# Kernel tuning notes

Hardware: AMD Instinct MI355X
Metric: run time of the kernel (lower is better)

## Reference

```python
import jax, jax.numpy as jnp
import numpy as np
import math

N_CELLS = 2048; HC_DIM = 11; HC_NODES = 2048
D = 1024; IN_DIM = 512; L = 2; H = 8; B = 2; HD = D // H
# XOR neighbor table: hypercube scatter-to-neighbor == gather-from-neighbor (involution)
NBR_WALK = jnp.asarray(np.arange(HC_NODES)[:, None] ^ (1 << np.arange(HC_DIM)))  # [Nn, hc_dim]
NB_INJ = min(HC_DIM, 6)
NB_FRUST = min(int(math.log2(N_CELLS)), 10)
FRUST_BITS = jnp.asarray(1 << np.arange(NB_FRUST))
N_MORPH = 48; N_FRUST_SAMPLES = min(N_CELLS, 128)


def _walk_step(amps, coin, x_mean):
    coined = jnp.einsum('ij,njd->nid', coin, amps)              # [Nn,2,D] complex
    new1 = coined[:, 1, :][NBR_WALK].sum(1) / HC_DIM            # XOR neighbor mix
    new = jnp.stack([coined[:, 0, :], new1], axis=1)
    new = new * jnp.exp(1j * (x_mean * 0.1))
    return new / (jnp.sqrt((jnp.abs(new) ** 2).sum()) + 1e-8)


def _inject(cells, amps):
    probs = (jnp.abs(amps) ** 2).sum((1, 2))
    probs = probs / (probs.sum() + 1e-8)
    ph = jnp.angle(amps.sum(1)).mean(-1)                        # [Nn]
    idx = jnp.arange(N_CELLS) % HC_NODES
    p = probs[idx]
    phc = ph[idx] * 0.3
    cells = cells * (0.8 + 0.4 * p)[:, None]
    c, s = jnp.cos(phc)[:, None], jnp.sin(phc)[:, None]
    h1, h2 = cells[:, :D // 2], cells[:, D // 2:]
    rot = jnp.concatenate([h1 * c - h2 * s, h1 * s + h2 * c], axis=1)
    cells = 0.5 * rot + 0.5 * cells
    nbr = idx[:, None] ^ (1 << jnp.arange(NB_INJ))              # [n_cells, 6]
    interf = ((p[:, None] - probs[nbr]) * 0.03).sum(1)
    return cells + interf[:, None]


def _frustration(cells, fsigns):
    # sequential in torch (cells[j] may already be updated for j<i) -> fori_loop
    def body(i, cells):
        j = i ^ FRUST_BITS
        valid = (j < N_CELLS).astype(cells.dtype)
        sign = fsigns[i] * fsigns[j] * valid
        infl = (sign[:, None] * cells[j]).sum(0)
        cnt = valid.sum()
        return cells.at[i].set(0.85 * cells[i] + 0.15 * infl / jnp.maximum(cnt, 1.0))
    return jax.lax.fori_loop(0, N_FRUST_SAMPLES, body, cells)


def _standing_wave(cells, step):
    i = jnp.arange(N_CELLS, dtype=cells.dtype)
    fwd = (step * 0.15) % N_CELLS
    bwd = (N_CELLS - step * 0.15) % N_CELLS
    amp = 1.0 / jnp.cosh((i - fwd) / 2) ** 2 + 1.0 / jnp.cosh((i - bwd) / 2) ** 2
    return cells * (1.0 + 0.03 * amp)[:, None]


def _morphism(cells):
    # torch hs[j] are views, so updates are visible sequentially -> fori_loop
    def body(i, cells):
        ms = jnp.tanh(cells[:N_MORPH] - cells[i]).sum(0) / (N_MORPH - 1)  # tanh(0)=0 handles j==i
        return cells.at[i].set(0.9 * cells[i] + 0.1 * ms)
    return jax.lax.fori_loop(0, N_MORPH, body, cells)


def _faction(cells, step, sync=0.15, debate=0.15, n_f=8):
    fsz = N_CELLS // n_f
    h = cells.reshape(n_f, fsz, D)
    h = (1 - sync) * h + sync * h.mean(1, keepdims=True)
    if step > 5:
        g = h.mean(1).mean(0)
        dc = max(1, fsz // 4)
        h = h.at[:, :dc].set((1 - debate) * h[:, :dc] + debate * g)
    return h.reshape(N_CELLS, D)


def _ln(x, g, b, eps=1e-5):
    mu = x.mean(-1, keepdims=True)
    v = ((x - mu) ** 2).mean(-1, keepdims=True)
    return (x - mu) / jnp.sqrt(v + eps) * g + b


def _update_cells(cells, amp_real, amp_imag, coin_real, coin_imag, fsigns, x, step):
    amps = amp_real + 1j * amp_imag
    coin = coin_real + 1j * coin_imag
    x_mean = x.mean()
    for _ in range(2):  # process() runs walk+inject twice
        amps = _walk_step(amps, coin, x_mean)
        cells = _inject(cells, amps)
    cells = _frustration(cells, fsigns)
    cells = _standing_wave(cells, step)
    if step % 3 == 0:
        cells = _morphism(cells)
    return _faction(cells, step)


def _forward(x, amp_real, amp_imag, coin_real, coin_imag, cell_embeddings, frustration_signs,
             w_in, b_in, attn_in_w, attn_in_b, attn_out_w, attn_out_b, ln_g, ln_b, w_out, b_out, step):
    upd = jax.lax.stop_gradient(_update_cells(
        cell_embeddings, amp_real, amp_imag, coin_real, coin_imag, frustration_signs, x, step))
    # straight-through: torch mutates .data in place, Parameter grad flows through updated values
    cells0 = cell_embeddings + jax.lax.stop_gradient(upd - cell_embeddings)
    x_proj = x @ w_in.T + b_in                                   # [B, D]
    cells = cells0[None] + x_proj[:, None] * 0.1                 # [B, S, D]
    tension = jnp.float32(0.0)
    for l in range(L):
        qkv = cells @ attn_in_w[l].T + attn_in_b[l]
        q, k, v = jnp.split(qkv, 3, axis=-1)
        q = q.reshape(B, N_CELLS, H, HD).transpose(0, 2, 1, 3)
        k = k.reshape(B, N_CELLS, H, HD).transpose(0, 2, 1, 3)
        v = v.reshape(B, N_CELLS, H, HD).transpose(0, 2, 1, 3)
        attn = jax.nn.softmax(jnp.einsum('bhqd,bhkd->bhqk', q, k) / math.sqrt(HD), axis=-1)
        out = jnp.einsum('bhqk,bhkd->bhqd', attn, v).transpose(0, 2, 1, 3).reshape(B, N_CELLS, D)
        out = out @ attn_out_w[l].T + attn_out_b[l]
        cells = _ln(cells + out, ln_g[l], ln_b[l])
        tension = tension + jnp.std(attn.mean(1), ddof=1)        # torch MHA averages heads; std unbiased
    tension = tension / L
    output = cells @ w_out.T + b_out                             # [B, S, IN_DIM]
    return output, tension


def setup_inputs():
    key = jax.random.key(0)
    ks = jax.random.split(key, 12)
    x = jax.random.normal(ks[0], (B, IN_DIM), jnp.float32)
    ar = jax.random.normal(ks[1], (HC_NODES, 2, D), jnp.float32) * 0.1
    ai = jax.random.normal(ks[2], (HC_NODES, 2, D), jnp.float32) * 0.1
    nrm = jnp.sqrt((ar ** 2 + ai ** 2).sum()) + 1e-8
    cells = jax.random.normal(ks[3], (N_CELLS, D), jnp.float32) * 0.1
    perm = jax.random.permutation(ks[4], N_CELLS)
    fsigns = jnp.ones(N_CELLS, jnp.float32).at[perm[:N_CELLS // 2]].set(-1.0)
    s = 1.0 / math.sqrt(D)
    return dict(
        x=x, amp_real=ar / nrm, amp_imag=ai / nrm,
        coin_real=jnp.array([[1.0, 1.0], [1.0, -1.0]], jnp.float32) / math.sqrt(2),
        coin_imag=jnp.zeros((2, 2), jnp.float32),
        cell_embeddings=cells, frustration_signs=fsigns,
        w_in=jax.random.normal(ks[5], (D, IN_DIM), jnp.float32) / math.sqrt(IN_DIM),
        b_in=jnp.zeros(D, jnp.float32),
        attn_in_w=jax.random.normal(ks[6], (L, 3 * D, D), jnp.float32) * s,
        attn_in_b=jnp.zeros((L, 3 * D), jnp.float32),
        attn_out_w=jax.random.normal(ks[7], (L, D, D), jnp.float32) * s,
        attn_out_b=jnp.zeros((L, D), jnp.float32),
        ln_g=jnp.ones((L, D), jnp.float32), ln_b=jnp.zeros((L, D), jnp.float32),
        w_out=jax.random.normal(ks[8], (IN_DIM, D), jnp.float32) * s,
        b_out=jnp.zeros(IN_DIM, jnp.float32),
        step=6)


def reference(x, amp_real, amp_imag, coin_real, coin_imag, cell_embeddings, frustration_signs,
              w_in, b_in, attn_in_w, attn_in_b, attn_out_w, attn_out_b, ln_g, ln_b, w_out, b_out, step):
    return _forward(x, amp_real, amp_imag, coin_real, coin_imag, cell_embeddings, frustration_signs,
                    w_in, b_in, attn_in_w, attn_in_b, attn_out_w, attn_out_b, ln_g, ln_b, w_out, b_out, step)
```

## Files before the change

kernel.cpp:

```cpp
#include <hip/hip_runtime.h>

#define U16 unsigned short

typedef short bf16x8 __attribute__((ext_vector_type(8)));
typedef float f32x4 __attribute__((ext_vector_type(4)));

__device__ __forceinline__ float bfp(const U16* p) { return __uint_as_float(((unsigned)(*p)) << 16); }
__device__ __forceinline__ U16 f2bf(float f) {
  unsigned u = __float_as_uint(f);
  u += 0x7FFFu + ((u >> 16) & 1u);
  return (U16)(u >> 16);
}
__device__ __forceinline__ float ldv(const void* p, long i, bool bf) {
  return bf ? bfp((const U16*)p + i) : ((const float*)p)[i];
}
__device__ __forceinline__ void gload_lds16(const U16* g, U16* l) {
  __builtin_amdgcn_global_load_lds((const __attribute__((address_space(1))) void*)g,
                                   (__attribute__((address_space(3))) void*)l, 16, 0, 0);
}


__global__ __launch_bounds__(256) void init_kernel(const void* __restrict__ x, const U16* __restrict__ lng,
                                                   float* __restrict__ scal) {
  __shared__ float red[256];
  __shared__ int fl;
  int t = threadIdx.x;
  if (t == 0) fl = (lng[0] != 0) ? 1 : 0;
  __syncthreads();
  bool bf = fl != 0;
  float s = 0.f;
  for (int i = t; i < 1024; i += 256) s += ldv(x, i, bf);
  red[t] = s; __syncthreads();
  for (int o = 128; o; o >>= 1) { if (t < o) red[t] += red[t + o]; __syncthreads(); }
  if (t == 0) { scal[0] = red[0] * (1.f / 1024.f); scal[16] = bf ? 1.f : 0.f; }
  else if (t < 64 && t != 16) scal[t] = 0.f;
}

__global__ __launch_bounds__(256) void walk_coined_kernel(const void* __restrict__ arv, const void* __restrict__ aiv,
                                                          float* __restrict__ cr, float* __restrict__ ci,
                                                          const void* __restrict__ coinR, const void* __restrict__ coinI,
                                                          const float* __restrict__ scal, int iter) {
  bool bf = scal[16] != 0.f;
  int id = blockIdx.x * 256 + threadIdx.x;
  int n = id >> 10, d = id & 1023;
  size_t b0 = (size_t)n * 2048 + d;
  float pre = 1.f;
  float a0r, a0i, a1r, a1i;
  if (iter == 0) {
    a0r = ldv(arv, b0, bf); a1r = ldv(arv, b0 + 1024, bf);
    a0i = ldv(aiv, b0, bf); a1i = ldv(aiv, b0 + 1024, bf);
  } else {
    pre = 1.f / (sqrtf(scal[iter]) + 1e-8f);
    const float* ar = (const float*)arv;
    const float* ai = (const float*)aiv;
    a0r = ar[b0]; a1r = ar[b0 + 1024]; a0i = ai[b0]; a1i = ai[b0 + 1024];
  }
  a0r *= pre; a0i *= pre; a1r *= pre; a1i *= pre;
  float c00r = ldv(coinR, 0, bf), c01r = ldv(coinR, 1, bf), c10r = ldv(coinR, 2, bf), c11r = ldv(coinR, 3, bf);
  float c00i = ldv(coinI, 0, bf), c01i = ldv(coinI, 1, bf), c10i = ldv(coinI, 2, bf), c11i = ldv(coinI, 3, bf);
  cr[b0]        = c00r * a0r - c00i * a0i + c01r * a1r - c01i * a1i;
  ci[b0]        = c00r * a0i + c00i * a0r + c01r * a1i + c01i * a1r;
  cr[b0 + 1024] = c10r * a0r - c10i * a0i + c11r * a1r - c11i * a1i;
  ci[b0 + 1024] = c10r * a0i + c10i * a0r + c11r * a1i + c11i * a1r;
}

__global__ __launch_bounds__(256) void walk_new_stats_kernel(const float* __restrict__ cr, const float* __restrict__ ci,
                                                             float* __restrict__ ar, float* __restrict__ ai,
                                                             const float* __restrict__ scal, float* __restrict__ scalw,
                                                             int slot, float* __restrict__ probs, float* __restrict__ ph) {
  __shared__ float r1[256], r2[256];
  int n = blockIdx.x, t = threadIdx.x;
  float th = scal[0] * 0.1f;
  float sn, cs; sincosf(th, &sn, &cs);
  float pacc = 0.f, phacc = 0.f;
  #pragma unroll
  for (int it = 0; it < 4; ++it) {
    int d = t + it * 256;
    size_t b0 = (size_t)n * 2048 + d;
    float n0r = cr[b0], n0i = ci[b0];
    float s1r = 0.f, s1i = 0.f;
    #pragma unroll
    for (int k = 0; k < 11; ++k) {
      size_t j = (size_t)(n ^ (1 << k)) * 2048 + 1024 + d;
      s1r += cr[j]; s1i += ci[j];
    }
    s1r *= (1.f / 11.f); s1i *= (1.f / 11.f);
    float o0r = n0r * cs - n0i * sn, o0i = n0r * sn + n0i * cs;
    float o1r = s1r * cs - s1i * sn, o1i = s1r * sn + s1i * cs;
    ar[b0] = o0r; ai[b0] = o0i; ar[b0 + 1024] = o1r; ai[b0 + 1024] = o1i;
    pacc += o0r * o0r + o0i * o0i + o1r * o1r + o1i * o1i;
    phacc += atan2f(o0i + o1i, o0r + o1r);
  }
  r1[t] = pacc; r2[t] = phacc; __syncthreads();
  for (int o = 128; o; o >>= 1) { if (t < o) { r1[t] += r1[t + o]; r2[t] += r2[t + o]; } __syncthreads(); }
  if (t == 0) { probs[n] = r1[0]; ph[n] = r2[0] * (1.f / 1024.f); atomicAdd(&scalw[slot], r1[0]); }
}

__global__ __launch_bounds__(256) void inject_cells_kernel(const void* __restrict__ cellsIn, float* __restrict__ cells,
                                                           const float* __restrict__ probs,
                                                           const float* __restrict__ ph, const float* __restrict__ scal,
                                                           int wslot, int useRaw) {
  bool bf = scal[16] != 0.f;
  int id = blockIdx.x * 256 + threadIdx.x;
  int c = id >> 9, d = id & 511;
  float invn = 1.f / (sqrtf(scal[wslot]) + 1e-8f);
  float inv2 = invn * invn;
  float denom = 1.f / (scal[wslot] * inv2 + 1e-8f);
  float psc = inv2 * denom;
  float p = probs[c] * psc;
  float interf = 0.f;
  #pragma unroll
  for (int j = 0; j < 6; ++j) interf += (p - probs[c ^ (1 << j)] * psc);
  interf *= 0.03f;
  float scale = 0.8f + 0.4f * p;
  float phc = ph[c] * 0.3f;
  float sn, cs; sincosf(phc, &sn, &cs);
  size_t base = (size_t)c * 1024 + d;
  float h1, h2;
  if (useRaw) { h1 = ldv(cellsIn, base, bf) * scale; h2 = ldv(cellsIn, base + 512, bf) * scale; }
  else        { h1 = cells[base] * scale;            h2 = cells[base + 512] * scale; }
  float r1 = h1 * cs - h2 * sn, r2 = h1 * sn + h2 * cs;
  cells[base]       = 0.5f * (r1 + h1) + interf;
  cells[base + 512] = 0.5f * (r2 + h2) + interf;
}

__global__ __launch_bounds__(64) void frustration_kernel(float* __restrict__ cells, const void* __restrict__ fs,
                                                         const float* __restrict__ scal) {
  bool bf = scal[16] != 0.f;
  int d = blockIdx.x;
  int l = threadIdx.x;
  float s0 = ldv(fs, l, bf);
  float s1 = ldv(fs, l + 64, bf);
  float w0 = s0 * cells[(size_t)l * 1024 + d];
  float w1 = s1 * cells[(size_t)(l + 64) * 1024 + d];
  float stat0 = 0.f, stat1 = 0.f;
  #pragma unroll
  for (int b = 7; b < 10; ++b) {
    int j0 = l ^ (1 << b);
    int j1 = (l + 64) ^ (1 << b);
    stat0 += ldv(fs, j0, bf) * cells[(size_t)j0 * 1024 + d];
    stat1 += ldv(fs, j1, bf) * cells[(size_t)j1 * 1024 + d];
  }
  #pragma unroll
  for (int i = 0; i < 128; ++i) {
    const int hi = i >> 6;
    const int li = i & 63;
    float vsrc = (hi == 0) ? w0 : w1;
    float voth = (hi == 0) ? w1 : w0;
    float acc = __shfl(vsrc, li ^ 1) + __shfl(vsrc, li ^ 2) + __shfl(vsrc, li ^ 4)
              + __shfl(vsrc, li ^ 8) + __shfl(vsrc, li ^ 16) + __shfl(vsrc, li ^ 32)
              + __shfl(voth, li);
    if (l == li) {
      if (hi == 0) w0 = 0.85f * w0 + 0.015f * (acc + stat0);
      else         w1 = 0.85f * w1 + 0.015f * (acc + stat1);
    }
  }
  cells[(size_t)l * 1024 + d]        = s0 * w0;
  cells[(size_t)(l + 64) * 1024 + d] = s1 * w1;
}

__global__ __launch_bounds__(256) void standing_kernel(float* __restrict__ cells, const int* __restrict__ stepp) {
  int id = blockIdx.x * 256 + threadIdx.x;
  int c = id >> 10;
  float st = (float)stepp[0] * 0.15f;
  float fwd = fmodf(st, 2048.f);
  float bwd = fmodf(2048.f - st, 2048.f);
  float fi = (float)c;
  float r1 = 1.f / coshf((fi - fwd) * 0.5f);
  float r2 = 1.f / coshf((fi - bwd) * 0.5f);
  cells[id] *= (1.f + 0.03f * (r1 * r1 + r2 * r2));
}

__global__ __launch_bounds__(64) void morphism_kernel(float* __restrict__ cells, const int* __restrict__ stepp) {
  if (stepp[0] % 3 != 0) return;
  int d = blockIdx.x;
  int l = threadIdx.x;
  float v = 0.f;
  if (l < 48) v = cells[(size_t)l * 1024 + d];
  for (int i = 0; i < 48; ++i) {
    float vi = __shfl(v, i);
    float x = v - vi;
    float e2 = __expf(2.f * x);
    float th = (l < 48) ? (1.f - 2.f / (e2 + 1.f)) : 0.f;
    th += __shfl_xor(th, 1);
    th += __shfl_xor(th, 2);
    th += __shfl_xor(th, 4);
    th += __shfl_xor(th, 8);
    th += __shfl_xor(th, 16);
    th += __shfl_xor(th, 32);
    if (l == i) v = 0.9f * v + (0.1f / 47.f) * th;
  }
  if (l < 48) cells[(size_t)l * 1024 + d] = v;
}

__global__ __launch_bounds__(256) void faction_mean_kernel(const float* __restrict__ cells, float* __restrict__ fmean) {
  int id = blockIdx.x * 256 + threadIdx.x;
  int f = id >> 10, d = id & 1023;
  float s = 0.f;
  for (int r = 0; r < 256; ++r) s += cells[(size_t)((f << 8) + r) * 1024 + d];
  fmean[id] = s * (1.f / 256.f);
}
__global__ __launch_bounds__(256) void faction_apply_kernel(float* __restrict__ cells, const float* __restrict__ fmean,
                                                            const int* __restrict__ stepp) {
  int id = blockIdx.x * 256 + threadIdx.x;
  int c = id >> 10, d = id & 1023;
  int f = c >> 8, r = c & 255;
  float v = 0.85f * cells[id] + 0.15f * fmean[f * 1024 + d];
  if (stepp[0] > 5 && r < 64) {
    float g = 0.f;
    #pragma unroll
    for (int ff = 0; ff < 8; ++ff) g += fmean[ff * 1024 + d];
    v = 0.85f * v + 0.15f * g * 0.125f;
  }
  cells[id] = v;
}

__global__ __launch_bounds__(256) void xproj_kernel(const void* __restrict__ x, const void* __restrict__ w_in,
                                                    const void* __restrict__ b_in, float* __restrict__ xp,
                                                    const float* __restrict__ scal) {
  bool bf = scal[16] != 0.f;
  int id = blockIdx.x * 256 + threadIdx.x;
  int b = id >> 10, o = id & 1023;
  float acc = ldv(b_in, o, bf);
  if (bf) {
    const U16* xr = (const U16*)x + b * 512;
    const U16* wr = (const U16*)w_in + (long)o * 512;
    for (int k = 0; k < 512; ++k) acc += bfp(xr + k) * bfp(wr + k);
  } else {
    const float* xr = (const float*)x + b * 512;
    const float* wr = (const float*)w_in + (long)o * 512;
    for (int k = 0; k < 512; ++k) acc += xr[k] * wr[k];
  }
  xp[id] = acc;
}

__global__ __launch_bounds__(256) void cellsB_kernel(const float* __restrict__ cells, const float* __restrict__ xp,
                                                     float* __restrict__ cellsB, U16* __restrict__ cellsB16) {
  int id = blockIdx.x * 256 + threadIdx.x;
  int b = id >> 21;
  int cd = id & ((1 << 21) - 1);
  int d = id & 1023;
  float v = cells[cd] + 0.1f * xp[(b << 10) + d];
  cellsB[id] = v;
  cellsB16[id] = f2bf(v);
}

__global__ __launch_bounds__(256) void wcvt_kernel(const void* __restrict__ W, long off,
                                                   U16* __restrict__ dst, int n4,
                                                   const float* __restrict__ scal) {
  if (scal[16] != 0.f) return;
  int id = blockIdx.x * 256 + threadIdx.x;
  if (id < n4) {
    const float* src = (const float*)W + off;
    float4 v = *(const float4*)&src[(size_t)id * 4];
    ushort4 o;
    o.x = f2bf(v.x); o.y = f2bf(v.y); o.z = f2bf(v.z); o.w = f2bf(v.w);
    *(ushort4*)&dst[(size_t)id * 4] = o;
  }
}

__global__ __launch_bounds__(256) void mfma_gemm_kernel(const U16* __restrict__ A16,
                                                        const void* __restrict__ Wv, long Woff,
                                                        const U16* __restrict__ W16s,
                                                        const void* __restrict__ biasv, long Boff,
                                                        void* __restrict__ Cout, int N, int mode,
                                                        const float* __restrict__ scal) {
  __shared__ U16 Al[3][4096];
  __shared__ U16 Wl[3][4096];
  bool bf = scal[16] != 0.f;
  const int K = 1024;
  const int NSTEP = 32;
  int t = threadIdx.x;
  int wv = t >> 6, l = t & 63;
  int n0 = blockIdx.x * 128, m0 = blockIdx.y * 128;
  int wmt = (wv & 1) * 4;
  int wnt = (wv >> 1) * 4;
  const U16* Wb = bf ? (const U16*)Wv + Woff : W16s;

  int fr0 = wv * 2, fr1 = fr0 + 1;
  const U16* asrc0 = A16 + (size_t)(m0 + fr0 * 16 + (l & 15)) * K + (l >> 4) * 8;
  const U16* asrc1 = A16 + (size_t)(m0 + fr1 * 16 + (l & 15)) * K + (l >> 4) * 8;
  const U16* wsrc0 = Wb  + (size_t)(n0 + fr0 * 16 + (l & 15)) * K + (l >> 4) * 8;
  const U16* wsrc1 = Wb  + (size_t)(n0 + fr1 * 16 + (l & 15)) * K + (l >> 4) * 8;

  auto stage = [&](int buf, int k0) {
    gload_lds16(asrc0 + k0, &Al[buf][fr0 * 512]);
    gload_lds16(asrc1 + k0, &Al[buf][fr1 * 512]);
    gload_lds16(wsrc0 + k0, &Wl[buf][fr0 * 512]);
    gload_lds16(wsrc1 + k0, &Wl[buf][fr1 * 512]);
  };

  f32x4 acc[4][4];
  #pragma unroll
  for (int i = 0; i < 4; ++i)
    #pragma unroll
    for (int j = 0; j < 4; ++j) acc[i][j] = (f32x4){0.f, 0.f, 0.f, 0.f};

  stage(0, 0);
  stage(1, 32);

  for (int s = 0; s < NSTEP; ++s) {
    if (s + 2 < NSTEP) {
      stage((s + 2) % 3, (s + 2) * 32);
      asm volatile("s_waitcnt vmcnt(8)" ::: "memory");
    } else if (s + 1 < NSTEP) {
      asm volatile("s_waitcnt vmcnt(4)" ::: "memory");
    } else {
      asm volatile("s_waitcnt vmcnt(0)" ::: "memory");
    }
    __builtin_amdgcn_s_barrier();
    asm volatile("" ::: "memory");
    int cb = s % 3;
    bf16x8 afr[4], bfr[4];
    #pragma unroll
    for (int i = 0; i < 4; ++i) afr[i] = *(const bf16x8*)&Al[cb][((wmt + i) * 64 + l) * 8];
    #pragma unroll
    for (int j = 0; j < 4; ++j) bfr[j] = *(const bf16x8*)&Wl[cb][((wnt + j) * 64 + l) * 8];
    #pragma unroll
    for (int i = 0; i < 4; ++i)
      #pragma unroll
      for (int j = 0; j < 4; ++j)
        acc[i][j] = __builtin_amdgcn_mfma_f32_16x16x32_bf16(afr[i], bfr[j], acc[i][j], 0, 0, 0);
    __builtin_amdgcn_s_barrier();
    asm volatile("" ::: "memory");
  }

  bool outBf = (mode == 1) || (mode == 2 && bf);
  int cl = l & 15, rq = l >> 4;
  #pragma unroll
  for (int j = 0; j < 4; ++j) {
    int n = n0 + (wnt + j) * 16 + cl;
    float bv = ldv(biasv, Boff + n, bf);
    #pragma unroll
    for (int i = 0; i < 4; ++i) {
      int mrow = m0 + (wmt + i) * 16 + rq * 4;
      #pragma unroll
      for (int r = 0; r < 4; ++r) {
        float v = acc[i][j][r] + bv;
        if (outBf) ((U16*)Cout)[(size_t)(mrow + r) * N + n] = f2bf(v);
        else       ((float*)Cout)[(size_t)(mrow + r) * N + n] = v;
      }
    }
  }
}

__global__ __launch_bounds__(256) void pack_kv_kernel(const U16* __restrict__ qkv,
                                                      U16* __restrict__ Kp, U16* __restrict__ Vp) {
  __shared__ U16 tile[64][132];
  int t = threadIdx.x;
  int kc = blockIdx.x, bh = blockIdx.y;
  int b = bh >> 3, h = bh & 7;
  size_t dstB = ((size_t)bh * 32 + kc) * 8192;
  if (blockIdx.z == 0) {
    int w = t >> 6, l = t & 63;
    int l16 = l & 15, quad = l >> 4;
    #pragma unroll
    for (int fi = 0; fi < 4; ++fi) {
      int f = w * 4 + fi;
      int nt = f >> 2, kf = f & 3;
      const U16* src = qkv + ((size_t)(b * 2048 + kc * 64 + nt * 16 + l16)) * 3072 + 1024 + h * 128 + kf * 32 + quad * 8;
      *(uint4*)(Kp + dstB + (size_t)f * 512 + l * 8) = *(const uint4*)src;
    }
  } else {
    int r = t >> 2, c0 = (t & 3) * 32;
    const U16* src = qkv + ((size_t)(b * 2048 + kc * 64 + r)) * 3072 + 2048 + h * 128 + c0;
    #pragma unroll
    for (int q = 0; q < 8; ++q)
      *(ushort4*)&tile[r][c0 + q * 4] = *(const ushort4*)(src + q * 4);
    __syncthreads();
    #pragma unroll
    for (int i = 0; i < 4; ++i) {
      int p = t + 256 * i;
      int g = p >> 6, l = p & 63;
      int l16 = l & 15, quad = l >> 4;
      int nt = g >> 1, kf = g & 1;
      U16 vals[8];
      #pragma unroll
      for (int j = 0; j < 8; ++j) vals[j] = tile[kf * 32 + quad * 8 + j][nt * 16 + l16];
      *(uint4*)(Vp + dstB + (size_t)g * 512 + l * 8) = *(const uint4*)vals;
    }
  }
}

__global__ __launch_bounds__(256) void zero_zg_kernel(float* __restrict__ zg) {
  int id = blockIdx.x * 256 + threadIdx.x;
  if (id < 294912) zg[id] = 0.f;
}

#define EHST 1040
#define EBST (8 * EHST)
__global__ __launch_bounds__(1024, 4) void attn_mfma_kernel(U16* __restrict__ qkv,
                                                            const U16* __restrict__ Kp, const U16* __restrict__ Vp,
                                                            float* __restrict__ O32a,
                                                            float* __restrict__ zg) {
  __shared__ U16 ebuf[2 * EBST];
  int t = threadIdx.x;
  int w16 = t >> 6;
  int h = w16 & 7;
  int l = t & 63;
  int l16 = l & 15, quad = l >> 4;
  int idx = blockIdx.x;
  int khalf = idx & 1;
  int b = (idx >> 1) & 1;
  int q0 = (idx >> 2) * 32;
  size_t rowB = (size_t)b * 2048;
  const float sc = 0.08838834764831845f;
  const int c0 = khalf * 32, cend = c0 + 32;

  if (w16 < 8) {
    const U16* KpB = Kp + (size_t)(b * 8 + h) * 262144;
    bf16x8 afr[2][4];
    #pragma unroll
    for (int s = 0; s < 2; ++s) {
      const U16* Qb = qkv + (rowB + q0 + s * 16 + l16) * 3072 + h * 128 + quad * 8;
      #pragma unroll
      for (int kf = 0; kf < 4; ++kf) afr[s][kf] = *(const bf16x8*)(Qb + kf * 32);
    }
    f32x4 gacc[2];
    gacc[0] = (f32x4){0.f, 0.f, 0.f, 0.f};
    gacc[1] = (f32x4){0.f, 0.f, 0.f, 0.f};
    float zacc[2][4] = {{0.f, 0.f, 0.f, 0.f}, {0.f, 0.f, 0.f, 0.f}};
    bf16x8 bK[2][4];

    auto kload = [&](int c) {
      int kc64 = c >> 1, nh = (c & 1) * 2;
      #pragma unroll
      for (int i = 0; i < 2; ++i)
        #pragma unroll
        for (int kf = 0; kf < 4; ++kf)
          bK[i][kf] = *(const bf16x8*)(KpB + (size_t)kc64 * 8192 + (size_t)((nh + i) * 4 + kf) * 512 + l * 8);
    };
    auto produce = [&](int c) {
      f32x4 sacc[2][2];
      #pragma unroll
      for (int s = 0; s < 2; ++s)
        #pragma unroll
        for (int i = 0; i < 2; ++i) {
          sacc[s][i] = (f32x4){0.f, 0.f, 0.f, 0.f};
          #pragma unroll
          for (int kf = 0; kf < 4; ++kf)
            sacc[s][i] = __builtin_amdgcn_mfma_f32_16x16x32_bf16(afr[s][kf], bK[i][kf], sacc[s][i], 0, 0, 0);
        }
      U16* eb = &ebuf[(c & 1) * EBST + h * EHST];
      #pragma unroll
      for (int s = 0; s < 2; ++s) {
        #pragma unroll
        for (int i = 0; i < 2; ++i) {
          int kq = i * 2 + (l16 >> 3);
          int j = l16 & 7;
          #pragma unroll
          for (int r = 0; r < 4; ++r) {
            float e = __expf(fminf(sacc[s][i][r] * sc, 30.f));
            zacc[s][r] += e;
            eb[s * 512 + kq * 128 + (quad * 4 + r) * 8 + j] = f2bf(e);
          }
        }
      }
    };

    kload(c0);
    produce(c0);
    if (c0 + 1 < cend) kload(c0 + 1);

    for (int c = c0; c < cend; ++c) {
      __syncthreads();
      if (c + 1 < cend) {
        produce(c + 1);
        if (c + 2 < cend) kload(c + 2);
      }
      const U16* gb = &ebuf[(c & 1) * EBST];
      #pragma unroll
      for (int s = 0; s < 2; ++s) {
        bf16x8 gfr = *(const bf16x8*)(gb + (size_t)(l & 7) * EHST + s * 512
                                      + (quad * 16 + h * 2 + ((l >> 3) & 1)) * 8);
        gacc[s] = __builtin_amdgcn_mfma_f32_16x16x32_bf16(gfr, gfr, gacc[s], 0, 0, 0);
      }
    }
    #pragma unroll
    for (int s = 0; s < 2; ++s)
      #pragma unroll
      for (int r = 0; r < 4; ++r) {
        float z = zacc[s][r];
        z += __shfl_xor(z, 1); z += __shfl_xor(z, 2);
        z += __shfl_xor(z, 4); z += __shfl_xor(z, 8);
        zacc[s][r] = z;
      }
    if (l16 == 0) {
      #pragma unroll
      for (int s = 0; s < 2; ++s)
        #pragma unroll
        for (int r = 0; r < 4; ++r) {
          size_t m = rowB + q0 + s * 16 + quad * 4 + r;
          atomicAdd(&zg[m * 8 + h], zacc[s][r]);
        }
    }
    {
      int h2 = l16 & 7, b2 = l16 >> 3;
      int a = quad >> 1;
      if (a == b2) {
        float* G = zg + 32768;
        #pragma unroll
        for (int s = 0; s < 2; ++s) {
          size_t m = rowB + q0 + s * 16 + h * 2 + a;
          #pragma unroll
          for (int r = 0; r < 4; ++r) {
            int h1 = (quad * 4 + r) & 7;
            atomicAdd(&G[m * 64 + h1 * 8 + h2], gacc[s][r]);
          }
        }
      }
    }
  } else {
    const U16* VpB = Vp + (size_t)(b * 8 + h) * 262144;
    f32x4 oacc[2][8];
    #pragma unroll
    for (int s = 0; s < 2; ++s)
      #pragma unroll
      for (int i = 0; i < 8; ++i) oacc[s][i] = (f32x4){0.f, 0.f, 0.f, 0.f};
    bf16x8 bV[8];

    auto vload = [&](int c) {
      int kc64 = c >> 1, vk = c & 1;
      #pragma unroll
      for (int nt = 0; nt < 8; ++nt)
        bV[nt] = *(const bf16x8*)(VpB + (size_t)kc64 * 8192 + (size_t)(nt * 2 + vk) * 512 + l * 8);
    };

    vload(c0);
    for (int c = c0; c < cend; ++c) {
      __syncthreads();
      const U16* eb = &ebuf[(c & 1) * EBST + h * EHST];
      #pragma unroll
      for (int s = 0; s < 2; ++s) {
        bf16x8 pfr = *(const bf16x8*)&eb[s * 512 + l * 8];
        #pragma unroll
        for (int nt = 0; nt < 8; ++nt)
          oacc[s][nt] = __builtin_amdgcn_mfma_f32_16x16x32_bf16(pfr, bV[nt], oacc[s][nt], 0, 0, 0);
      }
      if (c + 1 < cend) vload(c + 1);
    }
    #pragma unroll
    for (int s = 0; s < 2; ++s)
      #pragma unroll
      for (int r = 0; r < 4; ++r) {
        size_t m = rowB + q0 + s * 16 + quad * 4 + r;
        float* orow;
        if (khalf == 0) orow = O32a + m * 1024 + h * 128 + l16;
        else            orow = (float*)(qkv + m * 3072 + 1024) + h * 128 + l16;
        #pragma unroll
        for (int nt = 0; nt < 8; ++nt) orow[nt * 16] = oacc[s][nt][r];
      }
  }
}

__global__ __launch_bounds__(256) void attn_norm_kernel(const float* __restrict__ O32a, const U16* __restrict__ qkv,
                                                        const float* __restrict__ zg, U16* __restrict__ O16) {
  int id = blockIdx.x * 256 + threadIdx.x;
  int base = id * 4;
  int m = base >> 10, d = base & 1023;
  const float* ob = (const float*)(qkv + (size_t)m * 3072 + 1024);
  float4 a = *(const float4*)&O32a[base];
  float4 bv = *(const float4*)&ob[d];
  float inv = 1.f / zg[m * 8 + (d >> 7)];
  ushort4 o;
  o.x = f2bf((a.x + bv.x) * inv);
  o.y = f2bf((a.y + bv.y) * inv);
  o.z = f2bf((a.z + bv.z) * inv);
  o.w = f2bf((a.w + bv.w) * inv);
  *(ushort4*)&O16[base] = o;
}

__global__ __launch_bounds__(256) void gram_fin_kernel(const float* __restrict__ zg, float* __restrict__ scal, int slot) {
  __shared__ float red[256];
  int t = threadIdx.x;
  const float* G = zg + 32768;
  float s = 0.f;
  for (int i = blockIdx.x * 256 * 16 + t; i < (blockIdx.x + 1) * 256 * 16; i += 256) {
    int m = i >> 6, h1 = (i >> 3) & 7, h2 = i & 7;
    s += G[i] / (zg[m * 8 + h1] * zg[m * 8 + h2]);
  }
  red[t] = s; __syncthreads();
  for (int o = 128; o; o >>= 1) { if (t < o) red[t] += red[t + o]; __syncthreads(); }
  if (t == 0) atomicAdd(&scal[slot], red[0] * (1.f / 64.f) - (blockIdx.x == 0 ? 2.0f : 0.0f));
}

__global__ __launch_bounds__(256) void ln_kernel(float* __restrict__ cellsB, U16* __restrict__ cellsB16,
                                                 const float* __restrict__ proj,
                                                 const void* __restrict__ gv, const void* __restrict__ bv, long off,
                                                 const float* __restrict__ scal) {
  __shared__ float red[256];
  bool bf = scal[16] != 0.f;
  int row = blockIdx.x, t = threadIdx.x;
  size_t base = (size_t)row * 1024;
  int d = 4 * t;
  float4 cv = *(const float4*)&cellsB[base + d];
  float4 pv = *(const float4*)&proj[base + d];
  float v0 = cv.x + pv.x, v1 = cv.y + pv.y, v2 = cv.z + pv.z, v3 = cv.w + pv.w;
  red[t] = v0 + v1 + v2 + v3; __syncthreads();
  for (int o = 128; o; o >>= 1) { if (t < o) red[t] += red[t + o]; __syncthreads(); }
  float mu = red[0] * (1.f / 1024.f);
  __syncthreads();
  float d0 = v0 - mu, d1 = v1 - mu, d2 = v2 - mu, d3 = v3 - mu;
  red[t] = d0 * d0 + d1 * d1 + d2 * d2 + d3 * d3; __syncthreads();
  for (int o = 128; o; o >>= 1) { if (t < o) red[t] += red[t + o]; __syncthreads(); }
  float rstd = rsqrtf(red[0] * (1.f / 1024.f) + 1e-5f);
  float4 out;
  out.x = d0 * rstd * ldv(gv, off + d, bf)     + ldv(bv, off + d, bf);
  out.y = d1 * rstd * ldv(gv, off + d + 1, bf) + ldv(bv, off + d + 1, bf);
  out.z = d2 * rstd * ldv(gv, off + d + 2, bf) + ldv(bv, off + d + 2, bf);
  out.w = d3 * rstd * ldv(gv, off + d + 3, bf) + ldv(bv, off + d + 3, bf);
  *(float4*)&cellsB[base + d] = out;
  ushort4 ob;
  ob.x = f2bf(out.x); ob.y = f2bf(out.y); ob.z = f2bf(out.z); ob.w = f2bf(out.w);
  *(ushort4*)&cellsB16[base + d] = ob;
}

__global__ void tension_kernel(const float* __restrict__ scal, void* __restrict__ out) {
  bool bf = scal[16] != 0.f;
  float cnt = 8388608.f;
  float ten = 0.f;
  for (int l = 0; l < 2; ++l) {
    float v = scal[8 + l] / (cnt - 1.f);
    ten += sqrtf(fmaxf(v, 0.f));
  }
  ten *= 0.5f;
  if (bf) ((U16*)out)[2097152] = f2bf(ten);
  else    ((float*)out)[2097152] = ten;
}

extern "C" void kernel_launch(void* const* d_in, const int* in_sizes, int n_in,
                              void* d_out, int out_size, void* d_ws, size_t ws_size,
                              hipStream_t stream) {
  const void* X    = d_in[0];
  const void* AR   = d_in[1];
  const void* AI   = d_in[2];
  const void* CRc  = d_in[3];
  const void* CIc  = d_in[4];
  const void* CE   = d_in[5];
  const void* FS   = d_in[6];
  const void* WIN  = d_in[7];
  const void* BIN  = d_in[8];
  const void* AIW  = d_in[9];
  const void* AIB  = d_in[10];
  const void* AOW  = d_in[11];
  const void* AOB  = d_in[12];
  const void* LNG  = d_in[13];
  const void* LNB  = d_in[14];
  const void* WOUT = d_in[15];
  const void* BOUT = d_in[16];
  const int* STEP  = (const int*)d_in[17];

  float* ws = (float*)d_ws;
  float* scal  = ws;
  float* probs = ws + 64;
  float* ph    = ws + 64 + 2048;
  float* fmean = ws + 64 + 4096;
  float* xp    = ws + 64 + 12288;
  float* cells = ws + 16384;
  float* CB    = ws + 16384 + 2097152;
  float* ar = CB;
  float* ai = CB + 4194304;
  float* cr = CB + 8388608;
  float* ci = CB + 12582912;
  float* cellsB   = CB;
  U16*   qkv16    = (U16*)(CB + 4194304);
  float* proj     = CB + 4194304;
  float* O32a     = CB + 10485760;
  U16*   cellsB16 = (U16*)(CB + 12582912);
  U16*   Kp       = (U16*)(CB + 14680064);
  U16*   Vp       = (U16*)cells;
  U16*   O16      = Kp;
  float* zg       = (float*)d_out;
  U16*   Wd16     = (U16*)d_out;
  U16*   WOUT16   = (U16*)proj;

  init_kernel<<<1, 256, 0, stream>>>(X, (const U16*)LNG, scal);

  for (int w = 0; w < 2; ++w) {
    if (w == 0) walk_coined_kernel<<<8192, 256, 0, stream>>>(AR, AI, cr, ci, CRc, CIc, scal, 0);
    else        walk_coined_kernel<<<8192, 256, 0, stream>>>(ar, ai, cr, ci, CRc, CIc, scal, 1);
    walk_new_stats_kernel<<<2048, 256, 0, stream>>>(cr, ci, ar, ai, scal, scal, 1 + w, probs, ph);
    inject_cells_kernel<<<4096, 256, 0, stream>>>(w == 0 ? CE : (const void*)cells, cells,
                                                  probs, ph, scal, 1 + w, w == 0 ? 1 : 0);
  }
  frustration_kernel<<<1024, 64, 0, stream>>>(cells, FS, scal);
  standing_kernel<<<8192, 256, 0, stream>>>(cells, STEP);
  morphism_kernel<<<1024, 64, 0, stream>>>(cells, STEP);
  faction_mean_kernel<<<32, 256, 0, stream>>>(cells, fmean);
  faction_apply_kernel<<<8192, 256, 0, stream>>>(cells, fmean, STEP);

  xproj_kernel<<<8, 256, 0, stream>>>(X, WIN, BIN, xp, scal);
  cellsB_kernel<<<16384, 256, 0, stream>>>(cells, xp, cellsB, cellsB16);

  for (int l = 0; l < 2; ++l) {
    wcvt_kernel<<<3072, 256, 0, stream>>>(AIW, (long)l * 3072 * 1024, Wd16, 786432, scal);
    mfma_gemm_kernel<<<dim3(24, 32), 256, 0, stream>>>(cellsB16, AIW, (long)l * 3072 * 1024, Wd16,
                                                       AIB, (long)l * 3072, qkv16, 3072, 1, scal);
    pack_kv_kernel<<<dim3(32, 16, 2), 256, 0, stream>>>(qkv16, Kp, Vp);
    zero_zg_kernel<<<1152, 256, 0, stream>>>(zg);
    attn_mfma_kernel<<<256, 1024, 0, stream>>>(qkv16, Kp, Vp, O32a, zg);
    attn_norm_kernel<<<4096, 256, 0, stream>>>(O32a, qkv16, zg, O16);
    gram_fin_kernel<<<64, 256, 0, stream>>>(zg, scal, 8 + l);
    wcvt_kernel<<<1024, 256, 0, stream>>>(AOW, (long)l * 1024 * 1024, Wd16, 262144, scal);
    mfma_gemm_kernel<<<dim3(8, 32), 256, 0, stream>>>(O16, AOW, (long)l * 1024 * 1024, Wd16,
                                                      AOB, (long)l * 1024, proj, 1024, 0, scal);
    ln_kernel<<<4096, 256, 0, stream>>>(cellsB, cellsB16, proj, LNG, LNB, (long)l * 1024, scal);
  }
  wcvt_kernel<<<512, 256, 0, stream>>>(WOUT, 0, WOUT16, 131072, scal);
  mfma_gemm_kernel<<<dim3(4, 32), 256, 0, stream>>>(cellsB16, WOUT, 0, WOUT16,
                                                    BOUT, 0, d_out, 512, 2, scal);
  tension_kernel<<<1, 1, 0, stream>>>(scal, d_out);
}
```

Before: 781.7 us.

## Split attention keys into four chunks with atomic accumulation of outputs

The attention kernel now splits the key range into four quarters instead of two, doubling the grid to 512 blocks. Partial outputs are combined with float atomicAdd into a single buffer that is zeroed beforehand, instead of being written to two separate buffers (one of them aliasing the qkv region). The aim is more parallelism and better occupancy on the many-CU GPU. In exchange it adds atomic traffic, a larger zeroing pass over the full output buffer, and a nondeterministic summation order.

```diff
diff --git a/kernel.cpp b/kernel.cpp
--- a/kernel.cpp
+++ b/kernel.cpp
@@ -382,14 +382,15 @@
   }
 }
 
-__global__ __launch_bounds__(256) void zero_zg_kernel(float* __restrict__ zg) {
-  int id = blockIdx.x * 256 + threadIdx.x;
-  if (id < 294912) zg[id] = 0.f;
+__global__ __launch_bounds__(256) void zero_ozg_kernel(float* __restrict__ O32a, float* __restrict__ zg) {
+  int id = blockIdx.x * 256 + threadIdx.x;
+  if (id < 4194304) O32a[id] = 0.f;
+  else if (id < 4194304 + 294912) zg[id - 4194304] = 0.f;
 }
 
 #define EHST 1040
 #define EBST (8 * EHST)
-__global__ __launch_bounds__(1024, 4) void attn_mfma_kernel(U16* __restrict__ qkv,
+__global__ __launch_bounds__(1024, 4) void attn_mfma_kernel(const U16* __restrict__ qkv,
                                                             const U16* __restrict__ Kp, const U16* __restrict__ Vp,
                                                             float* __restrict__ O32a,
                                                             float* __restrict__ zg) {
@@ -400,12 +401,12 @@
   int l = t & 63;
   int l16 = l & 15, quad = l >> 4;
   int idx = blockIdx.x;
-  int khalf = idx & 1;
-  int b = (idx >> 1) & 1;
-  int q0 = (idx >> 2) * 32;
+  int kq4 = idx & 3;
+  int b = (idx >> 2) & 1;
+  int q0 = (idx >> 3) * 32;
   size_t rowB = (size_t)b * 2048;
   const float sc = 0.08838834764831845f;
-  const int c0 = khalf * 32, cend = c0 + 32;
+  const int c0 = kq4 * 16, cend = c0 + 16;
 
   if (w16 < 8) {
     const U16* KpB = Kp + (size_t)(b * 8 + h) * 262144;
@@ -544,29 +545,25 @@
       #pragma unroll
       for (int r = 0; r < 4; ++r) {
         size_t m = rowB + q0 + s * 16 + quad * 4 + r;
-        float* orow;
-        if (khalf == 0) orow = O32a + m * 1024 + h * 128 + l16;
-        else            orow = (float*)(qkv + m * 3072 + 1024) + h * 128 + l16;
+        float* orow = O32a + m * 1024 + h * 128 + l16;
         #pragma unroll
-        for (int nt = 0; nt < 8; ++nt) orow[nt * 16] = oacc[s][nt][r];
+        for (int nt = 0; nt < 8; ++nt) atomicAdd(&orow[nt * 16], oacc[s][nt][r]);
       }
   }
 }
 
-__global__ __launch_bounds__(256) void attn_norm_kernel(const float* __restrict__ O32a, const U16* __restrict__ qkv,
+__global__ __launch_bounds__(256) void attn_norm_kernel(const float* __restrict__ O32a,
                                                         const float* __restrict__ zg, U16* __restrict__ O16) {
   int id = blockIdx.x * 256 + threadIdx.x;
   int base = id * 4;
   int m = base >> 10, d = base & 1023;
-  const float* ob = (const float*)(qkv + (size_t)m * 3072 + 1024);
   float4 a = *(const float4*)&O32a[base];
-  float4 bv = *(const float4*)&ob[d];
   float inv = 1.f / zg[m * 8 + (d >> 7)];
   ushort4 o;
-  o.x = f2bf((a.x + bv.x) * inv);
-  o.y = f2bf((a.y + bv.y) * inv);
-  o.z = f2bf((a.z + bv.z) * inv);
-  o.w = f2bf((a.w + bv.w) * inv);
+  o.x = f2bf(a.x * inv);
+  o.y = f2bf(a.y * inv);
+  o.z = f2bf(a.z * inv);
+  o.w = f2bf(a.w * inv);
   *(ushort4*)&O16[base] = o;
 }
 
@@ -697,9 +694,9 @@
     mfma_gemm_kernel<<<dim3(24, 32), 256, 0, stream>>>(cellsB16, AIW, (long)l * 3072 * 1024, Wd16,
                                                        AIB, (long)l * 3072, qkv16, 3072, 1, scal);
     pack_kv_kernel<<<dim3(32, 16, 2), 256, 0, stream>>>(qkv16, Kp, Vp);
-    zero_zg_kernel<<<1152, 256, 0, stream>>>(zg);
-    attn_mfma_kernel<<<256, 1024, 0, stream>>>(qkv16, Kp, Vp, O32a, zg);
-    attn_norm_kernel<<<4096, 256, 0, stream>>>(O32a, qkv16, zg, O16);
+    zero_ozg_kernel<<<17536, 256, 0, stream>>>(O32a, zg);
+    attn_mfma_kernel<<<512, 1024, 0, stream>>>(qkv16, Kp, Vp, O32a, zg);
+    attn_norm_kernel<<<4096, 256, 0, stream>>>(O32a, zg, O16);
     gram_fin_kernel<<<64, 256, 0, stream>>>(zg, scal, 8 + l);
     wcvt_kernel<<<1024, 256, 0, stream>>>(AOW, (long)l * 1024 * 1024, Wd16, 262144, scal);
     mfma_gemm_kernel<<<dim3(8, 32), 256, 0, stream>>>(O16, AOW, (long)l * 1024 * 1024, Wd16,
```

After: 893.4 us. 1.14x slower.
